# Kernel tuning notes

Measured on AMD Instinct MI355X. Metric: run time of the kernel, lower is better.

Reference implementation:

```python
import jax, jax.numpy as jnp
import numpy as np

N_EMBD = 768
N_HEAD = 12
LN_EPS = 1e-5

def _ln(x, g, b):
    mu = jnp.mean(x, axis=-1, keepdims=True)
    var = jnp.mean(jnp.square(x - mu), axis=-1, keepdims=True)
    return (x - mu) * jax.lax.rsqrt(var + LN_EPS) * g + b

def setup_inputs() -> dict:
    key = jax.random.key(0)
    ks = jax.random.split(key, 16)
    C = N_EMBD
    s = lambda n: 0.02
    return {
        "x": jax.random.normal(ks[0], (4, 2048, C), jnp.float32),
        "ln1_g": jnp.ones((C,), jnp.float32),
        "ln1_b": jnp.zeros((C,), jnp.float32),
        "w_attn": jax.random.normal(ks[1], (C, 3 * C), jnp.float32) * s(C),
        "b_attn": jnp.zeros((3 * C,), jnp.float32),
        "w_proj": jax.random.normal(ks[2], (C, C), jnp.float32) * s(C),
        "b_proj": jnp.zeros((C,), jnp.float32),
        "ln2_g": jnp.ones((C,), jnp.float32),
        "ln2_b": jnp.zeros((C,), jnp.float32),
        "w_fc": jax.random.normal(ks[3], (C, 4 * C), jnp.float32) * s(C),
        "b_fc": jnp.zeros((4 * C,), jnp.float32),
        "w_fc2": jax.random.normal(ks[4], (4 * C, C), jnp.float32) * s(C),
        "b_fc2": jnp.zeros((C,), jnp.float32),
    }

def reference(x, ln1_g, ln1_b, w_attn, b_attn, w_proj, b_proj,
              ln2_g, ln2_b, w_fc, b_fc, w_fc2, b_fc2):
    B, T, C = x.shape
    H = N_HEAD
    hd = C // H
    # --- attention sublayer (pre-LN) ---
    h = _ln(x, ln1_g, ln1_b)
    qkv = h @ w_attn + b_attn                       # [B,T,3C]
    q, k, v = jnp.split(qkv, 3, axis=-1)
    q = q.reshape(B, T, H, hd).transpose(0, 2, 1, 3)  # [B,H,T,hd]
    k = k.reshape(B, T, H, hd).transpose(0, 2, 1, 3)
    v = v.reshape(B, T, H, hd).transpose(0, 2, 1, 3)
    aw = jnp.einsum("bhqd,bhkd->bhqk", q, k) / jnp.sqrt(jnp.float32(hd))
    mask = jnp.tril(jnp.ones((T, T), bool))
    aw = jnp.where(mask, aw, -jnp.inf)
    aw = jax.nn.softmax(aw, axis=-1)
    cv = jnp.einsum("bhqk,bhkd->bhqd", aw, v)       # [B,H,T,hd]
    cv = cv.transpose(0, 2, 1, 3).reshape(B, T, C)
    x = cv @ w_proj + b_proj + x
    # --- MLP sublayer (pre-LN) ---
    h = _ln(x, ln2_g, ln2_b)
    h = jax.nn.gelu(h @ w_fc + b_fc, approximate=True)
    x = h @ w_fc2 + b_fc2 + x
    return x
```

## Files before the change

kernel.cpp:

```cpp
#include <hip/hip_runtime.h>
#include <hip/hip_bf16.h>

typedef __attribute__((ext_vector_type(8))) short short8;
typedef __attribute__((ext_vector_type(4))) float f32x4;
typedef __attribute__((ext_vector_type(16))) float f32x16;
typedef __attribute__((ext_vector_type(4))) unsigned int u32x4;

__device__ __forceinline__ short bf16_bits(float f) {
    __hip_bfloat16 h = __float2bfloat16(f);
    return __builtin_bit_cast(short, h);
}

#define GLOAD_LDS16(g, l) __builtin_amdgcn_global_load_lds( \
    (const __attribute__((address_space(1))) void*)(g),     \
    (__attribute__((address_space(3))) void*)(l), 16, 0, 0)

__device__ __forceinline__ f32x16 mfma32(short8 a, short8 b, f32x16 c) {
    return __builtin_amdgcn_mfma_f32_32x32x16_bf16(a, b, c, 0, 0, 0);
}

__device__ __forceinline__ void half_swap(unsigned a, unsigned b,
                                          unsigned& x, unsigned& y) {
#if __has_builtin(__builtin_amdgcn_permlane32_swap)
    typedef __attribute__((ext_vector_type(2))) unsigned int uint2v;
    uint2v r = __builtin_amdgcn_permlane32_swap(a, b, false, false);
    x = r[0]; y = r[1];
#else
    unsigned bx_ = __shfl_xor((int)b, 32);
    unsigned ax_ = __shfl_xor((int)a, 32);
    int hi = (threadIdx.x & 63) >> 5;
    x = hi ? bx_ : a;
    y = hi ? b : ax_;
#endif
}

__global__ __launch_bounds__(256) void wcast_t(const float* __restrict__ w,
                                               short* __restrict__ wt, int K, int N) {
    __shared__ float tile[32][33];
    int n0 = blockIdx.x * 32, k0 = blockIdx.y * 32;
    int tx = threadIdx.x, ty = threadIdx.y;
#pragma unroll
    for (int i = 0; i < 32; i += 8)
        tile[ty + i][tx] = w[(size_t)(k0 + ty + i) * N + n0 + tx];
    __syncthreads();
#pragma unroll
    for (int i = 0; i < 32; i += 8)
        wt[(size_t)(n0 + ty + i) * K + k0 + tx] = bf16_bits(tile[tx][ty + i]);
}

__global__ __launch_bounds__(256) void ln_kernel(const float* __restrict__ x,
                                                 const float* __restrict__ g,
                                                 const float* __restrict__ bta,
                                                 short* __restrict__ out) {
    int row = blockIdx.x;
    const float* xr = x + (size_t)row * 768;
    int t = threadIdx.x;
    float v0 = xr[t], v1 = xr[t + 256], v2 = xr[t + 512];
    float s = v0 + v1 + v2;
#pragma unroll
    for (int o = 32; o; o >>= 1) s += __shfl_xor(s, o);
    __shared__ float red[8];
    int wid = t >> 6, lane = t & 63;
    if (lane == 0) red[wid] = s;
    __syncthreads();
    s = red[0] + red[1] + red[2] + red[3];
    float mu = s * (1.0f / 768.0f);
    float d0 = v0 - mu, d1 = v1 - mu, d2 = v2 - mu;
    float q = d0 * d0 + d1 * d1 + d2 * d2;
#pragma unroll
    for (int o = 32; o; o >>= 1) q += __shfl_xor(q, o);
    if (lane == 0) red[4 + wid] = q;
    __syncthreads();
    q = red[4] + red[5] + red[6] + red[7];
    float rstd = rsqrtf(q * (1.0f / 768.0f) + 1e-5f);
    short* orow = out + (size_t)row * 768;
    orow[t]       = bf16_bits(d0 * rstd * g[t]       + bta[t]);
    orow[t + 256] = bf16_bits(d1 * rstd * g[t + 256] + bta[t + 256]);
    orow[t + 512] = bf16_bits(d2 * rstd * g[t + 512] + bta[t + 512]);
}

#define BM 128
#define BN 128
#define BK 64

template <int EPI>
__global__ __launch_bounds__(256) void gemm_bt(const short* __restrict__ A,
                                               const short* __restrict__ BT,
                                               const float* __restrict__ bias,
                                               const float* __restrict__ res,
                                               void* __restrict__ outp,
                                               int M, int N, int K) {
    __shared__ short smem[2 * BM * BK];
    const int tid = threadIdx.x;
    const int lane = tid & 63;
    const int wid = tid >> 6;
    const int wr = wid >> 1, wc = wid & 1;
    const int laneb = lane & 15, laneh = lane >> 4;
    const int rowB0 = blockIdx.y * BM;
    const int colB0 = blockIdx.x * BN;

    f32x4 acc[4][4] = {};

    const char* gA = (const char*)(A + (size_t)rowB0 * K);
    const char* gB = (const char*)(BT + (size_t)colB0 * K);
    char* ldsA = (char*)smem;
    char* ldsB = (char*)(smem + BM * BK);
    const int wbase = tid & ~63;

    for (int k0 = 0; k0 < K; k0 += BK) {
        __syncthreads();
#pragma unroll
        for (int sub = 0; sub < 4; ++sub) {
            int idx = sub * 256 + tid;
            int row = idx >> 3;
            int inner = (idx & 7) << 4;
            int src = inner ^ ((row & 7) << 4);
            size_t gofs = (size_t)row * (K * 2) + (size_t)k0 * 2 + src;
            int lbase = (sub * 256 + wbase) * 16;
            GLOAD_LDS16(gA + gofs, ldsA + lbase);
            GLOAD_LDS16(gB + gofs, ldsB + lbase);
        }
        __syncthreads();
#pragma unroll
        for (int kk = 0; kk < 2; ++kk) {
            short8 af[4], bf[4];
#pragma unroll
            for (int m = 0; m < 4; ++m) {
                int r = wr * 64 + m * 16 + laneb;
                int kb = (kk * 64 + (laneh << 4)) ^ ((r & 7) << 4);
                af[m] = *(const short8*)(ldsA + r * 128 + kb);
            }
#pragma unroll
            for (int n = 0; n < 4; ++n) {
                int r = wc * 64 + n * 16 + laneb;
                int kb = (kk * 64 + (laneh << 4)) ^ ((r & 7) << 4);
                bf[n] = *(const short8*)(ldsB + r * 128 + kb);
            }
#pragma unroll
            for (int m = 0; m < 4; ++m)
#pragma unroll
                for (int n = 0; n < 4; ++n)
                    acc[m][n] = __builtin_amdgcn_mfma_f32_16x16x32_bf16(af[m], bf[n],
                                                                        acc[m][n], 0, 0, 0);
        }
    }

    const int r0 = rowB0 + wr * 64;
    const int c0 = colB0 + wc * 64;
#pragma unroll
    for (int m = 0; m < 4; ++m) {
#pragma unroll
        for (int n = 0; n < 4; ++n) {
            int col = c0 + n * 16 + laneb;
            float bv = bias[col];
#pragma unroll
            for (int j = 0; j < 4; ++j) {
                int row = r0 + m * 16 + (laneh << 2) + j;
                float v = acc[m][n][j] + bv;
                size_t o = (size_t)row * N + col;
                if constexpr (EPI == 1) {
                    ((float*)outp)[o] = v + res[o];
                } else if constexpr (EPI == 2) {
                    float u = 0.7978845608028654f * (v + 0.044715f * v * v * v);
                    ((short*)outp)[o] = bf16_bits(0.5f * v * (1.0f + tanhf(u)));
                } else {
                    ((short*)outp)[o] = bf16_bits(v);
                }
            }
        }
    }
}

__global__ __launch_bounds__(256) void build_vt(const short* __restrict__ qkv,
                                                short* __restrict__ vT) {
    constexpr int T = 2048, H = 12, LDQ = 2304;
    __shared__ short tile[32][33];
    int bh = blockIdx.z;
    int b = bh / H, h = bh % H;
    int t0 = blockIdx.x * 32, d0 = blockIdx.y * 32;
    int tx = threadIdx.x, ty = threadIdx.y;
    const short* src = qkv + (size_t)(b * T) * LDQ + 1536 + h * 64;
#pragma unroll
    for (int i = 0; i < 32; i += 8)
        tile[ty + i][tx] = src[(size_t)(t0 + ty + i) * LDQ + d0 + tx];
    __syncthreads();
    short* dst = vT + (size_t)bh * 64 * T;
#pragma unroll
    for (int i = 0; i < 32; i += 8)
        dst[(size_t)(d0 + ty + i) * T + t0 + tx] = tile[tx][ty + i];
}

__global__ __launch_bounds__(256) void attn_kernel(const short* __restrict__ qkv,
                                                   const short* __restrict__ vT,
                                                   short* __restrict__ cv) {
    constexpr int T = 2048, C = 768, H = 12, LDQ = 2304;
    constexpr int OST = 68;
    constexpr float SCL = 0.125f * 1.44269504088896f;
    __shared__ float ldsO[4 * 32 * OST];
    __shared__ float ldsM[128], ldsL[128];
    const int tid = threadIdx.x;
    const int lane = tid & 63;
    const int w = tid >> 6;
    const int l31 = lane & 31;
    const int hi = lane >> 5;

    const int g = blockIdx.x;
    const int xcd = g & 7;
    const int t = g >> 3;
    const int bh = xcd * 6 + (t >> 4);
    const int j = t & 15;
    const int b = bh / H, h = bh % H;

    const short* qbase = qkv + (size_t)(b * T) * LDQ + h * 64;
    const short* kbase = qbase + C;
    const short* vtb = vT + (size_t)bh * 64 * T;

#pragma unroll 1
    for (int pi = 0; pi < 4; ++pi) {
        int c;
        if (pi == 0)      c = j;
        else if (pi == 1) c = 63 - j;
        else if (pi == 2) c = 16 + j;
        else              c = 47 - j;
        const int q0 = c * 32;

        short8 qf[4];
        {
            const short* p = qbase + (size_t)(q0 + l31) * LDQ + hi * 8;
            qf[0] = *(const short8*)(p);
            qf[1] = *(const short8*)(p + 16);
            qf[2] = *(const short8*)(p + 32);
            qf[3] = *(const short8*)(p + 48);
        }

        f32x16 o0 = {}, o1 = {};
        float m = -3e38f, lsum = 0.f;

        for (int kt = w; kt <= c; kt += 4) {
            const int k0 = kt * 32;
            const short* kp = kbase + (size_t)(k0 + l31) * LDQ + hi * 8;
            short8 kf0 = *(const short8*)(kp);
            short8 kf1 = *(const short8*)(kp + 16);
            short8 kf2 = *(const short8*)(kp + 32);
            short8 kf3 = *(const short8*)(kp + 48);

            f32x16 s = {};
            s = mfma32(kf0, qf[0], s);
            s = mfma32(kf1, qf[1], s);
            s = mfma32(kf2, qf[2], s);
            s = mfma32(kf3, qf[3], s);

            const bool diag = (kt == c);
            float pmax = -3e38f;
#pragma unroll
            for (int r = 0; r < 16; ++r) {
                float v = s[r] * SCL;
                if (diag) {
                    int key = (r & 3) + 8 * (r >> 2) + 4 * hi;
                    if (key > l31) v = -3e38f;
                }
                s[r] = v;
                pmax = fmaxf(pmax, v);
            }
            pmax = fmaxf(pmax, __shfl_xor(pmax, 32));

            if (__any(pmax > m + 11.5f)) {
                float mn = fmaxf(m, pmax);
                float corr = exp2f(m - mn);
                lsum *= corr;
                m = mn;
#pragma unroll
                for (int r = 0; r < 16; ++r) {
                    float cr = __shfl(corr, (r & 3) + 8 * (r >> 2) + 4 * hi);
                    o0[r] *= cr;
                    o1[r] *= cr;
                }
            }

            float rs = 0.f;
#pragma unroll
            for (int r = 0; r < 16; ++r) {
                float p = exp2f(s[r] - m);
                s[r] = p;
                rs += p;
            }
            rs += __shfl_xor(rs, 32);
            lsum += rs;

            unsigned pk[8];
#pragma unroll
            for (int i = 0; i < 8; ++i)
                pk[i] = ((unsigned)(unsigned short)bf16_bits(s[2 * i + 1]) << 16) |
                        (unsigned short)bf16_bits(s[2 * i]);
            unsigned a0, a2, a1, a3, b0, b2, b1, b3;
            half_swap(pk[0], pk[2], a0, a2);
            half_swap(pk[1], pk[3], a1, a3);
            half_swap(pk[4], pk[6], b0, b2);
            half_swap(pk[5], pk[7], b1, b3);
            u32x4 w0v = {a0, a1, a2, a3};
            u32x4 w1v = {b0, b1, b2, b3};
            short8 pa0 = __builtin_bit_cast(short8, w0v);
            short8 pa1 = __builtin_bit_cast(short8, w1v);

            const short* vp0 = vtb + (size_t)l31 * T + k0 + hi * 8;
            const short* vp1 = vp0 + (size_t)32 * T;
            short8 v00 = *(const short8*)(vp0);
            short8 v01 = *(const short8*)(vp0 + 16);
            short8 v10 = *(const short8*)(vp1);
            short8 v11 = *(const short8*)(vp1 + 16);

            o0 = mfma32(pa0, v00, o0);
            o0 = mfma32(pa1, v01, o0);
            o1 = mfma32(pa0, v10, o1);
            o1 = mfma32(pa1, v11, o1);
        }

        float* myO = ldsO + w * 32 * OST;
#pragma unroll
        for (int r = 0; r < 16; ++r) {
            int q = (r & 3) + 8 * (r >> 2) + 4 * hi;
            myO[q * OST + l31] = o0[r];
            myO[q * OST + 32 + l31] = o1[r];
        }
        if (hi == 0) {
            ldsM[w * 32 + l31] = m;
            ldsL[w * 32 + l31] = lsum;
        }
        __syncthreads();

        {
            int qi = lane >> 3;
            int q = w * 8 + qi;
            int dj = (lane & 7) * 8;
            float mw[4];
#pragma unroll
            for (int u = 0; u < 4; ++u) mw[u] = ldsM[u * 32 + q];
            float M = fmaxf(fmaxf(mw[0], mw[1]), fmaxf(mw[2], mw[3]));
            float L = 0.f;
            f32x4 s0 = {}, s1 = {};
#pragma unroll
            for (int u = 0; u < 4; ++u) {
                float sc = exp2f(mw[u] - M);
                L += ldsL[u * 32 + q] * sc;
                const float* p = ldsO + u * 32 * OST + q * OST + dj;
                f32x4 a = *(const f32x4*)(p);
                f32x4 cc = *(const f32x4*)(p + 4);
#pragma unroll
                for (int jj = 0; jj < 4; ++jj) { s0[jj] += a[jj] * sc; s1[jj] += cc[jj] * sc; }
            }
            float inv = 1.0f / L;
            short8 ov;
#pragma unroll
            for (int jj = 0; jj < 4; ++jj) {
                ov[jj] = bf16_bits(s0[jj] * inv);
                ov[4 + jj] = bf16_bits(s1[jj] * inv);
            }
            short* dst = cv + (size_t)(b * T + q0 + q) * C + h * 64 + dj;
            *(short8*)dst = ov;
        }
        __syncthreads();
    }
}

extern "C" void kernel_launch(void* const* d_in, const int* in_sizes, int n_in,
                              void* d_out, int out_size, void* d_ws, size_t ws_size,
                              hipStream_t stream) {
    const float* x      = (const float*)d_in[0];
    const float* ln1_g  = (const float*)d_in[1];
    const float* ln1_b  = (const float*)d_in[2];
    const float* w_attn = (const float*)d_in[3];
    const float* b_attn = (const float*)d_in[4];
    const float* w_proj = (const float*)d_in[5];
    const float* b_proj = (const float*)d_in[6];
    const float* ln2_g  = (const float*)d_in[7];
    const float* ln2_b  = (const float*)d_in[8];
    const float* w_fc   = (const float*)d_in[9];
    const float* b_fc   = (const float*)d_in[10];
    const float* w_fc2  = (const float*)d_in[11];
    const float* b_fc2  = (const float*)d_in[12];

    char* ws = (char*)d_ws;
    short* wT_attn = (short*)(ws + 0);
    short* wT_proj = (short*)(ws + 3538944);
    short* wT_fc   = (short*)(ws + 4718592);
    short* wT_fc2  = (short*)(ws + 9437184);
    short* bufA    = (short*)(ws + 14155776);
    short* qkvb    = (short*)(ws + 26738688);
    short* vT      = (short*)(ws + 64487424);
    float* x1      = (float*)(ws + 77070336);

    dim3 blkT(32, 8);
    wcast_t<<<dim3(72, 24), blkT, 0, stream>>>(w_attn, wT_attn, 768, 2304);
    wcast_t<<<dim3(24, 24), blkT, 0, stream>>>(w_proj, wT_proj, 768, 768);
    wcast_t<<<dim3(96, 24), blkT, 0, stream>>>(w_fc, wT_fc, 768, 3072);
    wcast_t<<<dim3(24, 96), blkT, 0, stream>>>(w_fc2, wT_fc2, 3072, 768);

    ln_kernel<<<8192, 256, 0, stream>>>(x, ln1_g, ln1_b, bufA);
    gemm_bt<0><<<dim3(18, 64), 256, 0, stream>>>(bufA, wT_attn, b_attn, nullptr,
                                                 qkvb, 8192, 2304, 768);
    build_vt<<<dim3(64, 2, 48), blkT, 0, stream>>>(qkvb, vT);
    attn_kernel<<<dim3(768), 256, 0, stream>>>(qkvb, vT, bufA);
    gemm_bt<1><<<dim3(6, 64), 256, 0, stream>>>(bufA, wT_proj, b_proj, x,
                                                x1, 8192, 768, 768);
    ln_kernel<<<8192, 256, 0, stream>>>(x1, ln2_g, ln2_b, bufA);
    gemm_bt<2><<<dim3(24, 64), 256, 0, stream>>>(bufA, wT_fc, b_fc, nullptr,
                                                 qkvb, 8192, 3072, 768);
    gemm_bt<1><<<dim3(6, 64), 256, 0, stream>>>(qkvb, wT_fc2, b_fc2, x1,
                                                d_out, 8192, 768, 3072);
}
```

Measured before the change: 355.5 us.

## Double attention grid and halve LDS output buffer with two-pass merge

Each attention block now handles two balanced query tiles (c and 63-c) instead of four, and the launch grows from 768 to 1536 blocks to expose more parallelism. The LDS buffer for the cross-wave output merge is halved by writing and reducing the two 32-column halves of O in sequence, which lowers LDS use per block so more blocks can be resident. The cost is two extra barriers per tile, output stores shrink from 16 to 8 bytes per lane, and Q fragments are reloaded by more blocks.

```diff
diff --git a/kernel.cpp b/kernel.cpp
--- a/kernel.cpp
+++ b/kernel.cpp
@@ -194,7 +194,7 @@
                                                    const short* __restrict__ vT,
                                                    short* __restrict__ cv) {
     constexpr int T = 2048, C = 768, H = 12, LDQ = 2304;
-    constexpr int OST = 68;
+    constexpr int OST = 36;
     constexpr float SCL = 0.125f * 1.44269504088896f;
     __shared__ float ldsO[4 * 32 * OST];
     __shared__ float ldsM[128], ldsL[128];
@@ -207,8 +207,8 @@
     const int g = blockIdx.x;
     const int xcd = g & 7;
     const int t = g >> 3;
-    const int bh = xcd * 6 + (t >> 4);
-    const int j = t & 15;
+    const int bh = xcd * 6 + (t >> 5);
+    const int j = t & 31;
     const int b = bh / H, h = bh % H;
 
     const short* qbase = qkv + (size_t)(b * T) * LDQ + h * 64;
@@ -216,12 +216,8 @@
     const short* vtb = vT + (size_t)bh * 64 * T;
 
 #pragma unroll 1
-    for (int pi = 0; pi < 4; ++pi) {
-        int c;
-        if (pi == 0)      c = j;
-        else if (pi == 1) c = 63 - j;
-        else if (pi == 2) c = 16 + j;
-        else              c = 47 - j;
+    for (int pi = 0; pi < 2; ++pi) {
+        const int c = pi ? 63 - j : j;
         const int q0 = c * 32;
 
         short8 qf[4];
@@ -320,7 +316,6 @@
         for (int r = 0; r < 16; ++r) {
             int q = (r & 3) + 8 * (r >> 2) + 4 * hi;
             myO[q * OST + l31] = o0[r];
-            myO[q * OST + 32 + l31] = o1[r];
         }
         if (hi == 0) {
             ldsM[w * 32 + l31] = m;
@@ -328,35 +323,50 @@
         }
         __syncthreads();
 
+        const int q = w * 8 + (lane >> 3);
+        const int dj = (lane & 7) * 4;
+        float mw[4], M, inv;
         {
-            int qi = lane >> 3;
-            int q = w * 8 + qi;
-            int dj = (lane & 7) * 8;
-            float mw[4];
 #pragma unroll
             for (int u = 0; u < 4; ++u) mw[u] = ldsM[u * 32 + q];
-            float M = fmaxf(fmaxf(mw[0], mw[1]), fmaxf(mw[2], mw[3]));
+            M = fmaxf(fmaxf(mw[0], mw[1]), fmaxf(mw[2], mw[3]));
             float L = 0.f;
-            f32x4 s0 = {}, s1 = {};
+            f32x4 s0 = {};
 #pragma unroll
             for (int u = 0; u < 4; ++u) {
                 float sc = exp2f(mw[u] - M);
+                mw[u] = sc;
                 L += ldsL[u * 32 + q] * sc;
-                const float* p = ldsO + u * 32 * OST + q * OST + dj;
-                f32x4 a = *(const f32x4*)(p);
-                f32x4 cc = *(const f32x4*)(p + 4);
-#pragma unroll
-                for (int jj = 0; jj < 4; ++jj) { s0[jj] += a[jj] * sc; s1[jj] += cc[jj] * sc; }
-            }
-            float inv = 1.0f / L;
-            short8 ov;
-#pragma unroll
-            for (int jj = 0; jj < 4; ++jj) {
-                ov[jj] = bf16_bits(s0[jj] * inv);
-                ov[4 + jj] = bf16_bits(s1[jj] * inv);
-            }
+                f32x4 a = *(const f32x4*)(ldsO + (u * 32 + q) * OST + dj);
+#pragma unroll
+                for (int jj = 0; jj < 4; ++jj) s0[jj] += a[jj] * sc;
+            }
+            inv = 1.0f / L;
             short* dst = cv + (size_t)(b * T + q0 + q) * C + h * 64 + dj;
-            *(short8*)dst = ov;
+#pragma unroll
+            for (int jj = 0; jj < 4; ++jj) dst[jj] = bf16_bits(s0[jj] * inv);
+        }
+        __syncthreads();
+
+#pragma unroll
+        for (int r = 0; r < 16; ++r) {
+            int qq = (r & 3) + 8 * (r >> 2) + 4 * hi;
+            myO[qq * OST + l31] = o1[r];
+        }
+        __syncthreads();
+
+        {
+            f32x4 s1 = {};
+#pragma unroll
+            for (int u = 0; u < 4; ++u) {
+                float sc = mw[u];
+                f32x4 a = *(const f32x4*)(ldsO + (u * 32 + q) * OST + dj);
+#pragma unroll
+                for (int jj = 0; jj < 4; ++jj) s1[jj] += a[jj] * sc;
+            }
+            short* dst = cv + (size_t)(b * T + q0 + q) * C + h * 64 + 32 + dj;
+#pragma unroll
+            for (int jj = 0; jj < 4; ++jj) dst[jj] = bf16_bits(s1[jj] * inv);
         }
         __syncthreads();
     }
@@ -399,7 +409,7 @@
     gemm_bt<0><<<dim3(18, 64), 256, 0, stream>>>(bufA, wT_attn, b_attn, nullptr,
                                                  qkvb, 8192, 2304, 768);
     build_vt<<<dim3(64, 2, 48), blkT, 0, stream>>>(qkvb, vT);
-    attn_kernel<<<dim3(768), 256, 0, stream>>>(qkvb, vT, bufA);
+    attn_kernel<<<dim3(1536), 256, 0, stream>>>(qkvb, vT, bufA);
     gemm_bt<1><<<dim3(6, 64), 256, 0, stream>>>(bufA, wT_proj, b_proj, x,
                                                 x1, 8192, 768, 768);
     ln_kernel<<<8192, 256, 0, stream>>>(x1, ln2_g, ln2_b, bufA);
```

Result: faster. 345.8 us (-2.7%).
